# Optimization experiments

Hardware: AMD Instinct MI355X
Metric: run time of the kernel (lower is better)

Reference implementation:

```python
import jax, jax.numpy as jnp
import numpy as np

B, R, C, E, H = 2, 16, 512, 1024, 16
D = E // H  # head_dim = 64


def setup_inputs() -> dict:
    key = jax.random.key(0)
    ks = jax.random.split(key, 9)
    s = 1.0 / np.sqrt(E)
    return {
        "x": jax.random.normal(ks[0], (B, R, C, E), dtype=jnp.float32),
        "wq": jax.random.uniform(ks[1], (E, E), jnp.float32, -s, s),
        "bq": jax.random.uniform(ks[2], (E,), jnp.float32, -s, s),
        "wk": jax.random.uniform(ks[3], (E, E), jnp.float32, -s, s),
        "bk": jax.random.uniform(ks[4], (E,), jnp.float32, -s, s),
        "wv": jax.random.uniform(ks[5], (E, E), jnp.float32, -s, s),
        "bv": jax.random.uniform(ks[6], (E,), jnp.float32, -s, s),
        "wo": jax.random.uniform(ks[7], (E, E), jnp.float32, -s, s),
        "bo": jax.random.uniform(ks[8], (E,), jnp.float32, -s, s),
    }


def reference(x, wq, bq, wk, bk, wv, bv, wo, bo):
    b, r, c, e = x.shape
    # projections: [b,r,c,e] -> [b,r,h,c,d]
    def split_heads(t):
        return t.reshape(b, r, c, H, D).transpose(0, 1, 3, 2, 4)
    q = split_heads(x @ wq + bq)
    k = split_heads(x @ wk + bk)
    v = split_heads(x @ wv + bv)
    scale = 1.0 / jnp.sqrt(jnp.asarray(D, x.dtype))
    logits = jnp.einsum('brhqd,brhkd->brhqk', q, k) * scale
    probs = jax.nn.softmax(logits, axis=-1)
    ctx = jnp.einsum('brhqk,brhkd->brhqd', probs, v)
    ctx = ctx.transpose(0, 1, 3, 2, 4).reshape(b, r, c, e)
    return ctx @ wo + bo
```

## Files before the change

kernel.cpp:

```cpp
#include <hip/hip_runtime.h>
#include <hip/hip_bf16.h>
#include <hip/hip_fp16.h>
#include <math.h>

typedef _Float16 half8 __attribute__((ext_vector_type(8)));
typedef __attribute__((ext_vector_type(4))) float floatx4;

constexpr int Bc = 2, Rc = 16, Cc = 512, Ec = 1024, Hc = 16, Dc = 64;
#define QSCALE 0.180336880111120425f

__device__ inline void gl_lds16(const void* g, void* l) {
  __builtin_amdgcn_global_load_lds(
      (const __attribute__((address_space(1))) void*)g,
      (__attribute__((address_space(3))) void*)l, 16, 0, 0);
}
__device__ inline unsigned short f2h(float f) {
  __half h = __float2half_rn(f);
  return *(unsigned short*)&h;
}
__device__ inline unsigned int pack_h2(float lo, float hi) {
  __half2 p = __float22half2_rn(make_float2(lo, hi));
  return *(unsigned int*)&p;
}

__global__ __launch_bounds__(256) void cvt_x(const float* __restrict__ x,
                                             unsigned short* __restrict__ xh) {
  const size_t base = ((size_t)blockIdx.x * 256 + threadIdx.x) * 8;
  float4 a = *(const float4*)(x + base);
  float4 b = *(const float4*)(x + base + 4);
  uint4 o;
  o.x = pack_h2(a.x, a.y);
  o.y = pack_h2(a.z, a.w);
  o.z = pack_h2(b.x, b.y);
  o.w = pack_h2(b.z, b.w);
  *(uint4*)(xh + base) = o;
}

__global__ __launch_bounds__(256) void wprep(
    const float* __restrict__ w0, const float* __restrict__ w1,
    const float* __restrict__ w2, const float* __restrict__ w3,
    unsigned short* __restrict__ t0, unsigned short* __restrict__ t1,
    unsigned short* __restrict__ t2, unsigned short* __restrict__ t3) {
  __shared__ float tile[64][65];
  const int z = blockIdx.z;
  const float* W = (z == 0) ? w0 : (z == 1) ? w1 : (z == 2) ? w2 : w3;
  unsigned short* T = (z == 0) ? t0 : (z == 1) ? t1 : (z == 2) ? t2 : t3;
  const int tid = threadIdx.x;
  const int bk = blockIdx.x * 64, bn = blockIdx.y * 64;
#pragma unroll
  for (int p = 0; p < 16; ++p) {
    int idx = p * 256 + tid;
    int lk = idx >> 6, ln = idx & 63;
    tile[ln][lk] = W[(size_t)(bk + lk) * 1024 + bn + ln];
  }
  __syncthreads();
#pragma unroll
  for (int p = 0; p < 16; ++p) {
    int idx = p * 256 + tid;
    int ln = idx >> 6, lk = idx & 63;
    T[(size_t)(bn + ln) * 1024 + bk + lk] = f2h(tile[ln][lk]);
  }
}

#define STG(OP, BUF, KT, H)                                                   \
  {                                                                           \
    const unsigned short* gsp_ = (OP) ? Bb : Ab;                              \
    unsigned short* lb_ =                                                     \
        ((OP) ? Bs : As) + (BUF) * 16384 + (H) * 8192 + w * 1024;             \
    _Pragma("unroll") for (int l_ = 0; l_ < 2; ++l_)                          \
        gl_lds16(gsp_ + (size_t)((H) * 128 + srow + l_ * 8) * 1024 +          \
                     (KT) * 64 + goff,                                        \
                 lb_ + l_ * 512);                                             \
  }

#define DSRA(BUF, MH)                                                         \
  _Pragma("unroll") for (int i_ = 0; i_ < 4; ++i_) {                          \
    const unsigned short* p_ =                                                \
        As + (BUF) * 16384 + (wm + (MH) * 64 + i_ * 16 + lr) * 64;            \
    af[i_][0] = *(const half8*)(p_ + sw0);                                    \
    af[i_][1] = *(const half8*)(p_ + sw1);                                    \
  }

#define DSRB(BUF, NH)                                                         \
  _Pragma("unroll") for (int j_ = 0; j_ < 2; ++j_) {                          \
    const unsigned short* p_ =                                                \
        Bs + (BUF) * 16384 + (wn + (NH) * 32 + j_ * 16 + lr) * 64;            \
    bf[j_][0] = *(const half8*)(p_ + sw0);                                    \
    bf[j_][1] = *(const half8*)(p_ + sw1);                                    \
  }

#define MFMA16(MH, NH)                                                        \
  _Pragma("unroll") for (int i_ = 0; i_ < 4; ++i_)                            \
      _Pragma("unroll") for (int j_ = 0; j_ < 2; ++j_) {                      \
    acc[(MH)*4 + i_][(NH)*2 + j_] = __builtin_amdgcn_mfma_f32_16x16x32_f16(   \
        af[i_][0], bf[j_][0], acc[(MH)*4 + i_][(NH)*2 + j_], 0, 0, 0);        \
    acc[(MH)*4 + i_][(NH)*2 + j_] = __builtin_amdgcn_mfma_f32_16x16x32_f16(   \
        af[i_][1], bf[j_][1], acc[(MH)*4 + i_][(NH)*2 + j_], 0, 0, 0);        \
  }

#define WAIT_LGKM0                                                            \
  {                                                                           \
    asm volatile("s_waitcnt lgkmcnt(0)" ::: "memory");                        \
    __builtin_amdgcn_sched_barrier(0);                                        \
  }
#define WAIT_VM(N)                                                            \
  {                                                                           \
    asm volatile("s_waitcnt vmcnt(" #N ")" ::: "memory");                     \
    __builtin_amdgcn_sched_barrier(0);                                        \
  }

#define TILE(T, BUF, S12, S4, VM0)                                            \
  {                                                                           \
                                                                      \
    DSRA(BUF, 0);                                                             \
    DSRB(BUF, 0);                                                             \
    if (S12) {                                                                \
      STG(0, (BUF) ^ 1, (T) + 1, 1);                                          \
      STG(1, (BUF) ^ 1, (T) + 1, 0);                                          \
    }                                                                         \
    __builtin_amdgcn_s_barrier();                                             \
    WAIT_LGKM0;                                                               \
    __builtin_amdgcn_s_setprio(1);                                            \
    MFMA16(0, 0);                                                             \
    __builtin_amdgcn_s_setprio(0);                                            \
    __builtin_amdgcn_s_barrier();                                             \
    __builtin_amdgcn_sched_barrier(0);                                        \
                                                                      \
    DSRB(BUF, 1);                                                             \
    if (S12) { STG(1, (BUF) ^ 1, (T) + 1, 1); }                               \
    __builtin_amdgcn_s_barrier();                                             \
    WAIT_LGKM0;                                                               \
    __builtin_amdgcn_s_setprio(1);                                            \
    MFMA16(0, 1);                                                             \
    __builtin_amdgcn_s_setprio(0);                                            \
    __builtin_amdgcn_s_barrier();                                             \
    __builtin_amdgcn_sched_barrier(0);                                        \
                                                                      \
    DSRA(BUF, 1);                                                             \
    __builtin_amdgcn_s_barrier();                                             \
    WAIT_LGKM0;                                                               \
    __builtin_amdgcn_s_setprio(1);                                            \
    MFMA16(1, 1);                                                             \
    __builtin_amdgcn_s_setprio(0);                                            \
    __builtin_amdgcn_s_barrier();                                             \
    __builtin_amdgcn_sched_barrier(0);                                        \
                                                                      \
    DSRB(BUF, 0);                                                             \
    if (S4) { STG(0, BUF, (T) + 2, 0); }                                      \
    if (VM0) { WAIT_VM(0); } else { WAIT_VM(2); }                             \
    __builtin_amdgcn_s_barrier();                                             \
    WAIT_LGKM0;                                                               \
    __builtin_amdgcn_s_setprio(1);                                            \
    MFMA16(1, 0);                                                             \
    __builtin_amdgcn_s_setprio(0);                                            \
    __builtin_amdgcn_s_barrier();                                             \
    __builtin_amdgcn_sched_barrier(0);                                        \
  }

template <int MODE>
__global__ __launch_bounds__(512, 2) void gemm256(
    const unsigned short* __restrict__ gA, const unsigned short* __restrict__ gB,
    const float* __restrict__ bq, const float* __restrict__ bk,
    const float* __restrict__ bv, unsigned short* __restrict__ qout,
    unsigned short* __restrict__ kout, unsigned short* __restrict__ vout,
    float* __restrict__ fout, const float* __restrict__ bo) {
  __shared__ unsigned short As[2 * 16384];
  __shared__ unsigned short Bs[2 * 16384];
  const int tid = threadIdx.x;
  const int w = tid >> 6, ln = tid & 63;
  const int lr = ln & 15, quad = ln >> 4;
  const int wm = (w >> 2) * 128, wn = (w & 3) * 64;
  int bm, bn;
  if (MODE == 0) {
    const int swz = (blockIdx.x & 7) * 96 + (blockIdx.x >> 3);
    bm = (swz / 12) * 256;
    bn = (swz % 12) * 256;
  } else {
    const int swz = (blockIdx.x & 7) * 32 + (blockIdx.x >> 3);
    bm = (swz >> 2) * 256;
    bn = (swz & 3) * 256;
  }
  const unsigned short* Ab = gA + (size_t)bm * 1024;
  const unsigned short* Bb = gB + (size_t)bn * 1024;
  const int goff = (ln >> 3) * 1024 + (((ln & 7) ^ (ln >> 3)) << 3);
  const int srow = w * 16;
  const int sw0 = ((quad ^ (lr & 7)) << 3);
  const int sw1 = (((4 | quad) ^ (lr & 7)) << 3);

  floatx4 acc[8][4];
#pragma unroll
  for (int i = 0; i < 8; ++i)
#pragma unroll
    for (int j = 0; j < 4; ++j) acc[i][j] = (floatx4)(0.f);
  half8 af[4][2], bf[2][2];

  STG(0, 0, 0, 0);
  STG(0, 0, 0, 1);
  STG(1, 0, 0, 0);
  STG(1, 0, 0, 1);
  STG(0, 1, 1, 0);
  WAIT_VM(2);
  __builtin_amdgcn_s_barrier();
  __builtin_amdgcn_sched_barrier(0);

  for (int t = 0; t < 7; ++t) {
    const int T0 = 2 * t;
    TILE(T0, 0, 1, 1, 0);
    TILE(T0 + 1, 1, 1, 1, 0);
  }
  TILE(14, 0, 1, 0, 1);
  TILE(15, 1, 0, 0, 1);

  const int q4 = quad * 4;
  const bool odd = ln & 1;
  if constexpr (MODE == 0) {
    const int z = bn >> 10;
    const float* bias = (z == 0) ? bq : (z == 1) ? bk : bv;
    const int czb = (bn & 1023) + wn;
#pragma unroll
    for (int i = 0; i < 8; ++i) {
#pragma unroll
      for (int j = 0; j < 4; ++j) {
        const int colz = czb + j * 16 + lr;
        float v[4];
#pragma unroll
        for (int r = 0; r < 4; ++r) v[r] = acc[i][j][r] + bias[colz];
        const int m0 = bm + wm + i * 16 + q4;
        const int h = colz >> 6, d = colz & 63;
        const int brr = m0 >> 9, c0 = m0 & 511;
        const size_t hb = ((size_t)brr * 16 + h) * 32768;
        if (z == 2) {
          uint2 o;
          o.x = pack_h2(v[0], v[1]);
          o.y = pack_h2(v[2], v[3]);
          *(uint2*)(vout + hb + (size_t)d * 512 + c0) = o;
        } else {
          unsigned short* outp = (z == 0) ? qout : kout;
          if (z == 0) {
#pragma unroll
            for (int r = 0; r < 4; ++r) v[r] *= QSCALE;
          }
#pragma unroll
          for (int rp = 0; rp < 2; ++rp) {
            float a = v[2 * rp], b = v[2 * rp + 1];
            float ax = __shfl_xor(a, 1), bx = __shfl_xor(b, 1);
            unsigned int u = odd ? pack_h2(bx, b) : pack_h2(a, ax);
            const int c = c0 + 2 * rp + (odd ? 1 : 0);
            const int dd = d & ~1;
            *(unsigned int*)(outp + hb + (size_t)c * 64 + dd) = u;
          }
        }
      }
    }
  } else {
#pragma unroll
    for (int i = 0; i < 8; ++i)
#pragma unroll
      for (int j = 0; j < 4; ++j) {
        const int col = bn + wn + j * 16 + lr;
#pragma unroll
        for (int r = 0; r < 4; ++r) {
          const int m = bm + wm + i * 16 + q4 + r;
          fout[(size_t)m * 1024 + col] = acc[i][j][r] + bo[col];
        }
      }
  }
}

__global__ __launch_bounds__(256, 2) void attn_mfma(
    const unsigned short* __restrict__ Qh, const unsigned short* __restrict__ Kb,
    const unsigned short* __restrict__ Vt, unsigned short* __restrict__ Ctx) {
  __shared__ unsigned short Ks[128 * 64];
  __shared__ unsigned short Vs[64 * 128];
  __shared__ unsigned short Ps[128][136];

  const int t = threadIdx.x;
  const int w = t >> 6, ln = t & 63;
  const int lane15 = ln & 15, quad = ln >> 4;
  const bool odd = ln & 1;
  const int bh = blockIdx.x >> 2;
  const int qb = (blockIdx.x & 3) * 128;

  half8 qf[2][2];
  {
    const size_t qbase =
        ((size_t)bh * 512 + qb + w * 32 + lane15) * 64 + quad * 8;
#pragma unroll
    for (int i = 0; i < 2; ++i)
#pragma unroll
      for (int c = 0; c < 2; ++c)
        qf[i][c] = *(const half8*)(Qh + qbase + (size_t)i * 16 * 64 + c * 32);
  }

  floatx4 oacc[2][4];
#pragma unroll
  for (int i = 0; i < 2; ++i)
#pragma unroll
    for (int dj = 0; dj < 4; ++dj) oacc[i][dj] = (floatx4)(0.f);
  float lsum[2][4];
#pragma unroll
  for (int i = 0; i < 2; ++i)
#pragma unroll
    for (int r = 0; r < 4; ++r) lsum[i][r] = 0.f;

  const unsigned short* kgb = Kb + (size_t)bh * 32768;
  const unsigned short* vgb = Vt + (size_t)bh * 32768;

  for (int kt = 0; kt < 512; kt += 128) {
    __syncthreads();
    {
      const unsigned short* kq = kgb + (size_t)kt * 64;
#pragma unroll
      for (int p = 0; p < 4; ++p) {
        const int s = p * 256 + t;
        const int kr = s >> 3, kc16 = s & 7;
        gl_lds16(kq + kr * 64 + ((kc16 ^ (kr & 7)) << 3), (char*)Ks + s * 16);
        const int vr = s >> 4, vc16 = s & 15;
        gl_lds16(vgb + vr * 512 + kt + ((vc16 ^ (vr & 15)) << 3),
                 (char*)Vs + s * 16);
      }
    }
    __syncthreads();

    floatx4 sacc[2][8];
#pragma unroll
    for (int i = 0; i < 2; ++i)
#pragma unroll
      for (int j = 0; j < 8; ++j) sacc[i][j] = (floatx4)(0.f);
#pragma unroll
    for (int j = 0; j < 8; ++j) {
      const int krow = j * 16 + lane15;
      const unsigned short* kr = Ks + krow * 64;
      half8 kf0 = *(const half8*)(kr + ((quad ^ (krow & 7)) << 3));
      half8 kf1 = *(const half8*)(kr + (((4 + quad) ^ (krow & 7)) << 3));
#pragma unroll
      for (int i = 0; i < 2; ++i) {
        sacc[i][j] = __builtin_amdgcn_mfma_f32_16x16x32_f16(qf[i][0], kf0,
                                                            sacc[i][j], 0, 0, 0);
        sacc[i][j] = __builtin_amdgcn_mfma_f32_16x16x32_f16(qf[i][1], kf1,
                                                            sacc[i][j], 0, 0, 0);
      }
    }

#pragma unroll
    for (int i = 0; i < 2; ++i) {
#pragma unroll
      for (int rp = 0; rp < 2; ++rp) {
        const int rA = rp * 2, rB = rA + 1;
        const int row = w * 32 + i * 16 + quad * 4 + rA + (odd ? 1 : 0);
        unsigned short* prow = &Ps[row][lane15 & ~1];
#pragma unroll
        for (int j = 0; j < 8; ++j) {
          const float pA = exp2f(sacc[i][j][rA]);
          const float pB = exp2f(sacc[i][j][rB]);
          lsum[i][rA] += pA;
          lsum[i][rB] += pB;
          const float an = __shfl_xor(pA, 1);
          const float bn = __shfl_xor(pB, 1);
          const float lo = odd ? bn : pA;
          const float hi = odd ? pB : an;
          *(unsigned int*)(prow + j * 16) = pack_h2(lo, hi);
        }
      }
    }

#pragma unroll
    for (int kc = 0; kc < 4; ++kc) {
      half8 pa0 = *(const half8*)&Ps[w * 32 + lane15][kc * 32 + quad * 8];
      half8 pa1 = *(const half8*)&Ps[w * 32 + 16 + lane15][kc * 32 + quad * 8];
#pragma unroll
      for (int dj = 0; dj < 4; ++dj) {
        const int drow = dj * 16 + lane15;
        half8 vf = *(const half8*)(
            Vs + drow * 128 + (((kc * 4 + quad) ^ (drow & 15)) << 3));
        oacc[0][dj] = __builtin_amdgcn_mfma_f32_16x16x32_f16(pa0, vf,
                                                             oacc[0][dj], 0, 0, 0);
        oacc[1][dj] = __builtin_amdgcn_mfma_f32_16x16x32_f16(pa1, vf,
                                                             oacc[1][dj], 0, 0, 0);
      }
    }
  }

  float invl[2][4];
#pragma unroll
  for (int i = 0; i < 2; ++i)
#pragma unroll
    for (int r = 0; r < 4; ++r) {
      float ls = lsum[i][r];
#pragma unroll
      for (int off = 1; off < 16; off <<= 1) ls += __shfl_xor(ls, off);
      invl[i][r] = 1.f / ls;
    }
  const int br = bh >> 4, h = bh & 15;
  const size_t mbase = (size_t)br * 512 + qb + w * 32;
#pragma unroll
  for (int i = 0; i < 2; ++i)
#pragma unroll
    for (int dj = 0; dj < 4; ++dj) {
      const int e = h * 64 + dj * 16 + lane15;
      const int ee = e & ~1;
#pragma unroll
      for (int rp = 0; rp < 2; ++rp) {
        const int rA = 2 * rp, rB = rA + 1;
        float a = oacc[i][dj][rA] * invl[i][rA];
        float b = oacc[i][dj][rB] * invl[i][rB];
        float ax = __shfl_xor(a, 1), bx = __shfl_xor(b, 1);
        unsigned int u = odd ? pack_h2(bx, b) : pack_h2(a, ax);
        const size_t m = mbase + i * 16 + quad * 4 + rA + (odd ? 1 : 0);
        *(unsigned int*)(Ctx + m * 1024 + ee) = u;
      }
    }
}

extern "C" void kernel_launch(void* const* d_in, const int* in_sizes, int n_in,
                              void* d_out, int out_size, void* d_ws,
                              size_t ws_size, hipStream_t stream) {
  const float* x = (const float*)d_in[0];
  const float* wq = (const float*)d_in[1];
  const float* bq = (const float*)d_in[2];
  const float* wk = (const float*)d_in[3];
  const float* bk = (const float*)d_in[4];
  const float* wv = (const float*)d_in[5];
  const float* bv = (const float*)d_in[6];
  const float* wo = (const float*)d_in[7];
  const float* bo = (const float*)d_in[8];
  float* out = (float*)d_out;

  char* w = (char*)d_ws;
  const size_t MiB = 1ull << 20;
  unsigned short* qbuf = (unsigned short*)(w + 0 * MiB);
  unsigned short* kbuf = (unsigned short*)(w + 32 * MiB);
  unsigned short* vtb = (unsigned short*)(w + 64 * MiB);
  unsigned short* xh = (unsigned short*)(w + 96 * MiB);
  unsigned short* ctx = (unsigned short*)(w + 128 * MiB);
  unsigned short* wqh = (unsigned short*)(w + 160 * MiB);
  unsigned short* wkh = (unsigned short*)(w + 162 * MiB);
  unsigned short* wvh = (unsigned short*)(w + 164 * MiB);
  unsigned short* woh = (unsigned short*)(w + 166 * MiB);

  cvt_x<<<8192, 256, 0, stream>>>(x, xh);
  wprep<<<dim3(16, 16, 4), 256, 0, stream>>>(wq, wk, wv, wo, wqh, wkh, wvh,
                                             woh);

  gemm256<0><<<768, 512, 0, stream>>>(xh, wqh, bq, bk, bv, qbuf, kbuf, vtb,
                                      nullptr, nullptr);

  attn_mfma<<<2048, 256, 0, stream>>>(qbuf, kbuf, vtb, ctx);

  gemm256<1><<<256, 512, 0, stream>>>(ctx, woh, nullptr, nullptr, nullptr,
                                      nullptr, nullptr, nullptr, out, bo);
}
```

Before: 398.4 us.

## Restructure GEMM pipeline to prefetch two tiles ahead with split B fragments

Reworks the 256x256 GEMM main loop so global-to-LDS staging for tile T+2 is issued into the current buffer as each quarter of the tile is consumed, rather than staging T+1 into the other buffer. B fragments are kept in two register sets (bf0/bf1), so the last MFMA quarter reuses them without another LDS read or barrier. The prologue now fills both buffers up front. The aim is deeper prefetch and fewer LDS reads and barriers per tile. The cost is more registers and finer-grained staging whose correctness relies on the row partitioning and vmcnt accounting.

```diff
diff --git a/kernel.cpp b/kernel.cpp
--- a/kernel.cpp
+++ b/kernel.cpp
@@ -62,15 +62,22 @@
   }
 }
 
-#define STG(OP, BUF, KT, H)                                                   \
+#define STG_A(BUF, KT, MH)                                                    \
   {                                                                           \
-    const unsigned short* gsp_ = (OP) ? Bb : Ab;                              \
-    unsigned short* lb_ =                                                     \
-        ((OP) ? Bs : As) + (BUF) * 16384 + (H) * 8192 + w * 1024;             \
-    _Pragma("unroll") for (int l_ = 0; l_ < 2; ++l_)                          \
-        gl_lds16(gsp_ + (size_t)((H) * 128 + srow + l_ * 8) * 1024 +          \
-                     (KT) * 64 + goff,                                        \
-                 lb_ + l_ * 512);                                             \
+    _Pragma("unroll") for (int l_ = 0; l_ < 2; ++l_) {                        \
+      const int r0_ = l_ * 128 + (MH) * 64 + w * 8;                           \
+      gl_lds16(Ab + (size_t)r0_ * 1024 + (size_t)(KT) * 64 + goff,            \
+               As + (BUF) * 16384 + r0_ * 64);                                \
+    }                                                                         \
+  }
+
+#define STG_B(BUF, KT, NH)                                                    \
+  {                                                                           \
+    _Pragma("unroll") for (int l_ = 0; l_ < 2; ++l_) {                        \
+      const int r0_ = (w >> 1) * 64 + (NH) * 32 + ((w & 1) * 2 + l_) * 8;     \
+      gl_lds16(Bb + (size_t)r0_ * 1024 + (size_t)(KT) * 64 + goff,            \
+               Bs + (BUF) * 16384 + r0_ * 64);                                \
+    }                                                                         \
   }
 
 #define DSRA(BUF, MH)                                                         \
@@ -81,21 +88,21 @@
     af[i_][1] = *(const half8*)(p_ + sw1);                                    \
   }
 
-#define DSRB(BUF, NH)                                                         \
+#define DSRB(BUF, NH, DST)                                                    \
   _Pragma("unroll") for (int j_ = 0; j_ < 2; ++j_) {                          \
     const unsigned short* p_ =                                                \
         Bs + (BUF) * 16384 + (wn + (NH) * 32 + j_ * 16 + lr) * 64;            \
-    bf[j_][0] = *(const half8*)(p_ + sw0);                                    \
-    bf[j_][1] = *(const half8*)(p_ + sw1);                                    \
-  }
-
-#define MFMA16(MH, NH)                                                        \
+    DST[j_][0] = *(const half8*)(p_ + sw0);                                   \
+    DST[j_][1] = *(const half8*)(p_ + sw1);                                   \
+  }
+
+#define MFMA16(MH, NH, BF)                                                    \
   _Pragma("unroll") for (int i_ = 0; i_ < 4; ++i_)                            \
       _Pragma("unroll") for (int j_ = 0; j_ < 2; ++j_) {                      \
     acc[(MH)*4 + i_][(NH)*2 + j_] = __builtin_amdgcn_mfma_f32_16x16x32_f16(   \
-        af[i_][0], bf[j_][0], acc[(MH)*4 + i_][(NH)*2 + j_], 0, 0, 0);        \
+        af[i_][0], BF[j_][0], acc[(MH)*4 + i_][(NH)*2 + j_], 0, 0, 0);        \
     acc[(MH)*4 + i_][(NH)*2 + j_] = __builtin_amdgcn_mfma_f32_16x16x32_f16(   \
-        af[i_][1], bf[j_][1], acc[(MH)*4 + i_][(NH)*2 + j_], 0, 0, 0);        \
+        af[i_][1], BF[j_][1], acc[(MH)*4 + i_][(NH)*2 + j_], 0, 0, 0);        \
   }
 
 #define WAIT_LGKM0                                                            \
@@ -109,50 +116,51 @@
     __builtin_amdgcn_sched_barrier(0);                                        \
   }
 
-#define TILE(T, BUF, S12, S4, VM0)                                            \
+#define TILE(T, BUF, STAGE, ENDW)                                             \
   {                                                                           \
-                                                                      \
+                                                \
     DSRA(BUF, 0);                                                             \
-    DSRB(BUF, 0);                                                             \
-    if (S12) {                                                                \
-      STG(0, (BUF) ^ 1, (T) + 1, 1);                                          \
-      STG(1, (BUF) ^ 1, (T) + 1, 0);                                          \
-    }                                                                         \
+    DSRB(BUF, 0, bf0);                                                        \
     __builtin_amdgcn_s_barrier();                                             \
     WAIT_LGKM0;                                                               \
     __builtin_amdgcn_s_setprio(1);                                            \
-    MFMA16(0, 0);                                                             \
+    MFMA16(0, 0, bf0);                                                        \
     __builtin_amdgcn_s_setprio(0);                                            \
     __builtin_amdgcn_s_barrier();                                             \
     __builtin_amdgcn_sched_barrier(0);                                        \
-                                                                      \
-    DSRB(BUF, 1);                                                             \
-    if (S12) { STG(1, (BUF) ^ 1, (T) + 1, 1); }                               \
+                               \
+    DSRB(BUF, 1, bf1);                                                        \
+    if (STAGE) {                                                              \
+      STG_A(BUF, (T) + 2, 0);                                                 \
+      STG_B(BUF, (T) + 2, 0);                                                 \
+    }                                                                         \
     __builtin_amdgcn_s_barrier();                                             \
     WAIT_LGKM0;                                                               \
     __builtin_amdgcn_s_setprio(1);                                            \
-    MFMA16(0, 1);                                                             \
+    MFMA16(0, 1, bf1);                                                        \
     __builtin_amdgcn_s_setprio(0);                                            \
     __builtin_amdgcn_s_barrier();                                             \
     __builtin_amdgcn_sched_barrier(0);                                        \
-                                                                      \
+                                         \
     DSRA(BUF, 1);                                                             \
+    if (STAGE) { STG_B(BUF, (T) + 2, 1); }                                    \
     __builtin_amdgcn_s_barrier();                                             \
     WAIT_LGKM0;                                                               \
     __builtin_amdgcn_s_setprio(1);                                            \
-    MFMA16(1, 1);                                                             \
+    MFMA16(1, 0, bf0);                                                        \
     __builtin_amdgcn_s_setprio(0);                                            \
     __builtin_amdgcn_s_barrier();                                             \
     __builtin_amdgcn_sched_barrier(0);                                        \
-                                                                      \
-    DSRB(BUF, 0);                                                             \
-    if (S4) { STG(0, BUF, (T) + 2, 0); }                                      \
-    if (VM0) { WAIT_VM(0); } else { WAIT_VM(2); }                             \
-    __builtin_amdgcn_s_barrier();                                             \
-    WAIT_LGKM0;                                                               \
+                \
+    if (STAGE) { STG_A(BUF, (T) + 2, 1); }                                    \
     __builtin_amdgcn_s_setprio(1);                                            \
-    MFMA16(1, 0);                                                             \
+    MFMA16(1, 1, bf1);                                                        \
     __builtin_amdgcn_s_setprio(0);                                            \
+    if (ENDW == 0) {                                                          \
+      WAIT_VM(8);                                                             \
+    } else if (ENDW == 1) {                                                   \
+      WAIT_VM(0);                                                             \
+    }                                                                         \
     __builtin_amdgcn_s_barrier();                                             \
     __builtin_amdgcn_sched_barrier(0);                                        \
   }
@@ -183,7 +191,6 @@
   const unsigned short* Ab = gA + (size_t)bm * 1024;
   const unsigned short* Bb = gB + (size_t)bn * 1024;
   const int goff = (ln >> 3) * 1024 + (((ln & 7) ^ (ln >> 3)) << 3);
-  const int srow = w * 16;
   const int sw0 = ((quad ^ (lr & 7)) << 3);
   const int sw1 = (((4 | quad) ^ (lr & 7)) << 3);
 
@@ -192,24 +199,26 @@
   for (int i = 0; i < 8; ++i)
 #pragma unroll
     for (int j = 0; j < 4; ++j) acc[i][j] = (floatx4)(0.f);
-  half8 af[4][2], bf[2][2];
-
-  STG(0, 0, 0, 0);
-  STG(0, 0, 0, 1);
-  STG(1, 0, 0, 0);
-  STG(1, 0, 0, 1);
-  STG(0, 1, 1, 0);
-  WAIT_VM(2);
+  half8 af[4][2], bf0[2][2], bf1[2][2];
+
+  STG_A(0, 0, 0);
+  STG_A(0, 0, 1);
+  STG_B(0, 0, 0);
+  STG_B(0, 0, 1);
+  STG_A(1, 1, 0);
+  STG_A(1, 1, 1);
+  STG_B(1, 1, 0);
+  STG_B(1, 1, 1);
+  WAIT_VM(8);
   __builtin_amdgcn_s_barrier();
   __builtin_amdgcn_sched_barrier(0);
 
   for (int t = 0; t < 7; ++t) {
-    const int T0 = 2 * t;
-    TILE(T0, 0, 1, 1, 0);
-    TILE(T0 + 1, 1, 1, 1, 0);
-  }
-  TILE(14, 0, 1, 0, 1);
-  TILE(15, 1, 0, 0, 1);
+    TILE(2 * t, 0, 1, 0);
+    TILE(2 * t + 1, 1, 1, 0);
+  }
+  TILE(14, 0, 0, 1);
+  TILE(15, 1, 0, 2);
 
   const int q4 = quad * 4;
   const bool odd = ln & 1;
```

Result: faster. 387.5 us (-2.7%).

## Restructure GEMM main loop into 4-stage K=32 pipeline with register double-buffering

Applied to the files above, without the earlier changes.

Replaces the 2-buffer K=64 tile schedule, which used four barrier-separated MFMA sub-phases and XOR-swizzled LDS, with a 4-buffer ring of K=32 slices. Each step issues the global-to-LDS loads for the slice three ahead, reads the next slice's fragments into a second register set, then runs 32 MFMAs on the current set. This cuts the barriers and lgkm waits per K-block and overlaps LDS reads with MFMA work. In exchange it drops the LDS swizzle, which risks bank conflicts on the 64-byte row stride, and doubles fragment registers, which may pressure occupancy at 512 threads x 2 blocks.

```diff
diff --git a/kernel.cpp b/kernel.cpp
--- a/kernel.cpp
+++ b/kernel.cpp
@@ -62,99 +62,48 @@
   }
 }
 
-#define STG(OP, BUF, KT, H)                                                   \
-  {                                                                           \
-    const unsigned short* gsp_ = (OP) ? Bb : Ab;                              \
-    unsigned short* lb_ =                                                     \
-        ((OP) ? Bs : As) + (BUF) * 16384 + (H) * 8192 + w * 1024;             \
-    _Pragma("unroll") for (int l_ = 0; l_ < 2; ++l_)                          \
-        gl_lds16(gsp_ + (size_t)((H) * 128 + srow + l_ * 8) * 1024 +          \
-                     (KT) * 64 + goff,                                        \
-                 lb_ + l_ * 512);                                             \
-  }
-
-#define DSRA(BUF, MH)                                                         \
-  _Pragma("unroll") for (int i_ = 0; i_ < 4; ++i_) {                          \
-    const unsigned short* p_ =                                                \
-        As + (BUF) * 16384 + (wm + (MH) * 64 + i_ * 16 + lr) * 64;            \
-    af[i_][0] = *(const half8*)(p_ + sw0);                                    \
-    af[i_][1] = *(const half8*)(p_ + sw1);                                    \
-  }
-
-#define DSRB(BUF, NH)                                                         \
-  _Pragma("unroll") for (int j_ = 0; j_ < 2; ++j_) {                          \
-    const unsigned short* p_ =                                                \
-        Bs + (BUF) * 16384 + (wn + (NH) * 32 + j_ * 16 + lr) * 64;            \
-    bf[j_][0] = *(const half8*)(p_ + sw0);                                    \
-    bf[j_][1] = *(const half8*)(p_ + sw1);                                    \
-  }
-
-#define MFMA16(MH, NH)                                                        \
-  _Pragma("unroll") for (int i_ = 0; i_ < 4; ++i_)                            \
-      _Pragma("unroll") for (int j_ = 0; j_ < 2; ++j_) {                      \
-    acc[(MH)*4 + i_][(NH)*2 + j_] = __builtin_amdgcn_mfma_f32_16x16x32_f16(   \
-        af[i_][0], bf[j_][0], acc[(MH)*4 + i_][(NH)*2 + j_], 0, 0, 0);        \
-    acc[(MH)*4 + i_][(NH)*2 + j_] = __builtin_amdgcn_mfma_f32_16x16x32_f16(   \
-        af[i_][1], bf[j_][1], acc[(MH)*4 + i_][(NH)*2 + j_], 0, 0, 0);        \
-  }
-
-#define WAIT_LGKM0                                                            \
-  {                                                                           \
-    asm volatile("s_waitcnt lgkmcnt(0)" ::: "memory");                        \
-    __builtin_amdgcn_sched_barrier(0);                                        \
-  }
 #define WAIT_VM(N)                                                            \
   {                                                                           \
     asm volatile("s_waitcnt vmcnt(" #N ")" ::: "memory");                     \
     __builtin_amdgcn_sched_barrier(0);                                        \
   }
 
-#define TILE(T, BUF, S12, S4, VM0)                                            \
+#define STG_AB(SBUF, KT)                                                      \
   {                                                                           \
-                                                                      \
-    DSRA(BUF, 0);                                                             \
-    DSRB(BUF, 0);                                                             \
-    if (S12) {                                                                \
-      STG(0, (BUF) ^ 1, (T) + 1, 1);                                          \
-      STG(1, (BUF) ^ 1, (T) + 1, 0);                                          \
+    _Pragma("unroll") for (int l_ = 0; l_ < 2; ++l_) {                        \
+      const int r0_ = l_ * 128 + w * 16;                                      \
+      gl_lds16(Ab + (size_t)r0_ * 1024 + glan + (size_t)(KT) * 32,            \
+               As + (SBUF) * 8192 + r0_ * 32);                                \
+      gl_lds16(Bb + (size_t)r0_ * 1024 + glan + (size_t)(KT) * 32,            \
+               Bs + (SBUF) * 8192 + r0_ * 32);                                \
     }                                                                         \
-    __builtin_amdgcn_s_barrier();                                             \
-    WAIT_LGKM0;                                                               \
-    __builtin_amdgcn_s_setprio(1);                                            \
-    MFMA16(0, 0);                                                             \
-    __builtin_amdgcn_s_setprio(0);                                            \
-    __builtin_amdgcn_s_barrier();                                             \
-    __builtin_amdgcn_sched_barrier(0);                                        \
-                                                                      \
-    DSRB(BUF, 1);                                                             \
-    if (S12) { STG(1, (BUF) ^ 1, (T) + 1, 1); }                               \
-    __builtin_amdgcn_s_barrier();                                             \
-    WAIT_LGKM0;                                                               \
-    __builtin_amdgcn_s_setprio(1);                                            \
-    MFMA16(0, 1);                                                             \
-    __builtin_amdgcn_s_setprio(0);                                            \
-    __builtin_amdgcn_s_barrier();                                             \
-    __builtin_amdgcn_sched_barrier(0);                                        \
-                                                                      \
-    DSRA(BUF, 1);                                                             \
-    __builtin_amdgcn_s_barrier();                                             \
-    WAIT_LGKM0;                                                               \
-    __builtin_amdgcn_s_setprio(1);                                            \
-    MFMA16(1, 1);                                                             \
-    __builtin_amdgcn_s_setprio(0);                                            \
-    __builtin_amdgcn_s_barrier();                                             \
-    __builtin_amdgcn_sched_barrier(0);                                        \
-                                                                      \
-    DSRB(BUF, 0);                                                             \
-    if (S4) { STG(0, BUF, (T) + 2, 0); }                                      \
-    if (VM0) { WAIT_VM(0); } else { WAIT_VM(2); }                             \
-    __builtin_amdgcn_s_barrier();                                             \
-    WAIT_LGKM0;                                                               \
-    __builtin_amdgcn_s_setprio(1);                                            \
-    MFMA16(1, 0);                                                             \
-    __builtin_amdgcn_s_setprio(0);                                            \
-    __builtin_amdgcn_s_barrier();                                             \
-    __builtin_amdgcn_sched_barrier(0);                                        \
+  }
+
+#define DSR(NBUF, FA, FB)                                                     \
+  {                                                                           \
+    _Pragma("unroll") for (int i_ = 0; i_ < 8; ++i_) FA[i_] =                 \
+        *(const half8*)&As[(NBUF) * 8192 + (wm + i_ * 16 + lr) * 32 + qk];    \
+    _Pragma("unroll") for (int j_ = 0; j_ < 4; ++j_) FB[j_] =                 \
+        *(const half8*)&Bs[(NBUF) * 8192 + (wn + j_ * 16 + lr) * 32 + qk];    \
+  }
+
+#define MFMA32(FA, FB)                                                        \
+  _Pragma("unroll") for (int i_ = 0; i_ < 8; ++i_)                            \
+      _Pragma("unroll") for (int j_ = 0; j_ < 4; ++j_) acc[i_][j_] =          \
+          __builtin_amdgcn_mfma_f32_16x16x32_f16(FA[i_], FB[j_],              \
+                                                 acc[i_][j_], 0, 0, 0);
+
+#define TSTEP(NBUF, SBUF, KT, FA, FB, NFA, NFB, STGE, NXTE, VMW)              \
+  {                                                                           \
+    if (STGE) STG_AB(SBUF, KT);                                               \
+    if (NXTE) DSR(NBUF, NFA, NFB);                                            \
+    MFMA32(FA, FB);                                                           \
+    if ((VMW) == 1) { WAIT_VM(4); }                                           \
+    if ((VMW) == 2) { WAIT_VM(0); }                                           \
+    if ((VMW) != 3) {                                                         \
+      __builtin_amdgcn_s_barrier();                                           \
+      __builtin_amdgcn_sched_barrier(0);                                      \
+    }                                                                         \
   }
 
 template <int MODE>
@@ -164,11 +113,12 @@
     const float* __restrict__ bv, unsigned short* __restrict__ qout,
     unsigned short* __restrict__ kout, unsigned short* __restrict__ vout,
     float* __restrict__ fout, const float* __restrict__ bo) {
-  __shared__ unsigned short As[2 * 16384];
-  __shared__ unsigned short Bs[2 * 16384];
+  __shared__ unsigned short As[4 * 8192];
+  __shared__ unsigned short Bs[4 * 8192];
   const int tid = threadIdx.x;
   const int w = tid >> 6, ln = tid & 63;
   const int lr = ln & 15, quad = ln >> 4;
+  const int qk = quad * 8;
   const int wm = (w >> 2) * 128, wn = (w & 3) * 64;
   int bm, bn;
   if (MODE == 0) {
@@ -182,34 +132,34 @@
   }
   const unsigned short* Ab = gA + (size_t)bm * 1024;
   const unsigned short* Bb = gB + (size_t)bn * 1024;
-  const int goff = (ln >> 3) * 1024 + (((ln & 7) ^ (ln >> 3)) << 3);
-  const int srow = w * 16;
-  const int sw0 = ((quad ^ (lr & 7)) << 3);
-  const int sw1 = (((4 | quad) ^ (lr & 7)) << 3);
+  const int glan = (ln >> 2) * 1024 + (ln & 3) * 8;
 
   floatx4 acc[8][4];
 #pragma unroll
   for (int i = 0; i < 8; ++i)
 #pragma unroll
     for (int j = 0; j < 4; ++j) acc[i][j] = (floatx4)(0.f);
-  half8 af[4][2], bf[2][2];
-
-  STG(0, 0, 0, 0);
-  STG(0, 0, 0, 1);
-  STG(1, 0, 0, 0);
-  STG(1, 0, 0, 1);
-  STG(0, 1, 1, 0);
-  WAIT_VM(2);
+  half8 fa0[8], fb0[4], fa1[8], fb1[4];
+
+  STG_AB(0, 0);
+  STG_AB(1, 1);
+  STG_AB(2, 2);
+  WAIT_VM(4);
   __builtin_amdgcn_s_barrier();
   __builtin_amdgcn_sched_barrier(0);
-
-  for (int t = 0; t < 7; ++t) {
-    const int T0 = 2 * t;
-    TILE(T0, 0, 1, 1, 0);
-    TILE(T0 + 1, 1, 1, 1, 0);
-  }
-  TILE(14, 0, 1, 0, 1);
-  TILE(15, 1, 0, 0, 1);
+  DSR(0, fa0, fb0);
+
+  for (int tt = 0; tt < 7; ++tt) {
+    const int k4 = tt * 4;
+    TSTEP(1, 3, k4 + 3, fa0, fb0, fa1, fb1, 1, 1, 1);
+    TSTEP(2, 0, k4 + 4, fa1, fb1, fa0, fb0, 1, 1, 1);
+    TSTEP(3, 1, k4 + 5, fa0, fb0, fa1, fb1, 1, 1, 1);
+    TSTEP(0, 2, k4 + 6, fa1, fb1, fa0, fb0, 1, 1, 1);
+  }
+  TSTEP(1, 3, 31, fa0, fb0, fa1, fb1, 1, 1, 1);
+  TSTEP(2, 0, 0, fa1, fb1, fa0, fb0, 0, 1, 2);
+  TSTEP(3, 0, 0, fa0, fb0, fa1, fb1, 0, 1, 3);
+  TSTEP(0, 0, 0, fa1, fb1, fa0, fb0, 0, 0, 3);
 
   const int q4 = quad * 4;
   const bool odd = ln & 1;
```

Result: no change. 394.3 us (-1.0%).
